# Kernel optimization log

Measured on AMD Instinct MI355X. Metric: run time of the kernel, lower is better.

The kernel has to match this reference:

```python
import jax, jax.numpy as jnp
import numpy as np

STRIDES = (8, 16, 32, 64, 128)
LEVEL_HW = ((128, 160), (64, 80), (32, 40), (16, 20), (8, 10))
IMG_H, IMG_W = 1024, 1280
B, NUM_CLASSES = 16, 20
SCORE_THR, IOU_THR, MAX_DET = 0.05, 0.6, 1000


def _coords_all():
    # coords_fmap2orig for every level, concatenated -> [N, 2] (x, y)
    cs = []
    for (h, w), s in zip(LEVEL_HW, STRIDES):
        sx = jnp.arange(w, dtype=jnp.float32) * s + s // 2
        sy = jnp.arange(h, dtype=jnp.float32) * s + s // 2
        yy, xx = jnp.meshgrid(sy, sx, indexing='ij')
        cs.append(jnp.stack([xx.reshape(-1), yy.reshape(-1)], -1))
    return jnp.concatenate(cs, 0)


def _reshape_cat(levels):
    # list of [B,C,h,w] -> [B, sum(h*w), C]
    return jnp.concatenate(
        [p.transpose(0, 2, 3, 1).reshape(p.shape[0], -1, p.shape[1]) for p in levels], 1)


def _decode(cls_l, cnt_l, reg_l, coords):
    cls = jax.nn.sigmoid(_reshape_cat(cls_l))           # [B,N,C]
    cnt = jax.nn.sigmoid(_reshape_cat(cnt_l))[..., 0]   # [B,N]
    reg = _reshape_cat(reg_l)                           # [B,N,4] ltrb
    scores = jnp.sqrt(jnp.max(cls, -1) * cnt)           # add_centerness + sqrt
    classes = jnp.argmax(cls, -1) + 1
    boxes = jnp.concatenate([coords[None] - reg[..., :2], coords[None] + reg[..., 2:]], -1)
    return scores, classes, boxes


def _nms_keep(boxes, scores, classes, valid):
    # masked greedy per-class NMS on fixed size M; returns keep mask [M]
    boxes = jax.lax.stop_gradient(boxes)
    scores = jax.lax.stop_gradient(scores)
    maxc = jnp.max(jnp.where(valid[:, None], boxes, 0.0))
    b = boxes + (classes.astype(boxes.dtype) * (maxc + 1.0))[:, None]  # class offsets
    order = jnp.argsort(-jnp.where(valid, scores, -jnp.inf))
    b = b[order]
    v = valid[order]
    x1, y1, x2, y2 = b[:, 0], b[:, 1], b[:, 2], b[:, 3]
    areas = (x2 - x1 + 1.0) * (y2 - y1 + 1.0)
    iw = jnp.clip(jnp.minimum(x2[:, None], x2[None, :]) - jnp.maximum(x1[:, None], x1[None, :]) + 1.0, 0.0)
    ih = jnp.clip(jnp.minimum(y2[:, None], y2[None, :]) - jnp.maximum(y1[:, None], y1[None, :]) + 1.0, 0.0)
    inter = iw * ih
    iou = inter / (areas[:, None] + areas[None, :] - inter)
    M = boxes.shape[0]

    def body(i, carry):
        keep, sup = carry
        k = v[i] & (~sup[i])
        keep = keep.at[i].set(k)
        sup = sup | (k & (iou[i] > IOU_THR))
        return keep, sup

    keep_s, _ = jax.lax.fori_loop(0, M, body, (jnp.zeros(M, bool), jnp.zeros(M, bool)))
    return jnp.zeros(M, bool).at[order].set(keep_s)


def _forward(args):
    cls_r, cnt_r, reg_r = args[0:5], args[5:10], args[10:15]
    cls_i, cnt_i, reg_i = args[15:20], args[20:25], args[25:30]
    coords = _coords_all()
    s_r, c_r, b_r = _decode(cls_r, cnt_r, reg_r, coords)
    s_i, c_i, b_i = _decode(cls_i, cnt_i, reg_i, coords)
    scores = jnp.concatenate([s_r, s_i], 1)   # [B, 2N]
    classes = jnp.concatenate([c_r, c_i], 1)
    boxes = jnp.concatenate([b_r, b_i], 1)
    top_s, top_i = jax.lax.top_k(scores, MAX_DET)
    top_c = jnp.take_along_axis(classes, top_i, 1)
    top_b = jnp.take_along_axis(boxes, top_i[..., None], 1)
    valid = top_s >= SCORE_THR
    keep = jax.vmap(_nms_keep)(top_b, top_s, top_c, valid)
    # ClipBoxes: clamp to image bounds
    top_b = jnp.maximum(top_b, 0.0)
    xs = jnp.minimum(top_b[..., 0::2], IMG_W - 1.0)
    ys = jnp.minimum(top_b[..., 1::2], IMG_H - 1.0)
    top_b = jnp.stack([xs[..., 0], ys[..., 0], xs[..., 1], ys[..., 1]], -1)
    kf = keep.astype(top_s.dtype)
    return top_s * kf, top_c * keep, top_b * kf[..., None], keep


def setup_inputs() -> dict:
    key = jax.random.key(0)
    chans = {'cls': NUM_CLASSES, 'cnt': 1, 'reg': 4}
    inp = {}
    i = 0
    for mod in ('r', 'i'):
        for kind in ('cls', 'cnt', 'reg'):
            for l, (h, w) in enumerate(LEVEL_HW):
                k = jax.random.fold_in(key, i); i += 1
                inp[f'{kind}_{mod}_{l}'] = jax.random.normal(k, (B, chans[kind], h, w), jnp.float32)
    return inp


def reference(cls_r_0, cls_r_1, cls_r_2, cls_r_3, cls_r_4,
              cnt_r_0, cnt_r_1, cnt_r_2, cnt_r_3, cnt_r_4,
              reg_r_0, reg_r_1, reg_r_2, reg_r_3, reg_r_4,
              cls_i_0, cls_i_1, cls_i_2, cls_i_3, cls_i_4,
              cnt_i_0, cnt_i_1, cnt_i_2, cnt_i_3, cnt_i_4,
              reg_i_0, reg_i_1, reg_i_2, reg_i_3, reg_i_4):
    args = [cls_r_0, cls_r_1, cls_r_2, cls_r_3, cls_r_4,
            cnt_r_0, cnt_r_1, cnt_r_2, cnt_r_3, cnt_r_4,
            reg_r_0, reg_r_1, reg_r_2, reg_r_3, reg_r_4,
            cls_i_0, cls_i_1, cls_i_2, cls_i_3, cls_i_4,
            cnt_i_0, cnt_i_1, cnt_i_2, cnt_i_3, cnt_i_4,
            reg_i_0, reg_i_1, reg_i_2, reg_i_3, reg_i_4]
    return _forward(args)
```

## Files before the change

### kernel.cpp

```cpp
#include <hip/hip_runtime.h>
#include <hip/hip_bf16.h>

typedef unsigned long long u64;
typedef unsigned int u32;

#define NTOT    54560
#define NMOD    27280
#define BATCH   16
#define KPAD    1024
#define MAXD    1000
#define NBIN    16384
#define CANDCAP 6144
#define NLDSPOS 25600

struct Ptrs { const float* p[30]; };

constexpr size_t SZ_KEY   = (size_t)BATCH * NTOT * 8;
constexpr size_t SZ_TOPK  = (size_t)BATCH * KPAD * 8;
constexpr size_t SZ_TRAW  = (size_t)BATCH * KPAD * 16;
constexpr size_t SZ_T1    = (size_t)BATCH * KPAD * 4;
constexpr size_t SZ_MAXC  = (size_t)BATCH * 32 * 4;
constexpr size_t SZ_VALID = (size_t)BATCH * 32 * 4;
constexpr size_t SZ_MASK  = (size_t)BATCH * KPAD * 32 * 4;

constexpr size_t OFF_KEY    = 0;
constexpr size_t OFF_TOPK   = OFF_KEY   + SZ_KEY;
constexpr size_t OFF_TRAW   = OFF_TOPK  + SZ_TOPK;
constexpr size_t OFF_TSCORE = OFF_TRAW  + SZ_TRAW;
constexpr size_t OFF_TCLSF  = OFF_TSCORE+ SZ_T1;
constexpr size_t OFF_MAXC   = OFF_TCLSF + SZ_T1;
constexpr size_t OFF_VALID  = OFF_MAXC  + SZ_MAXC;
constexpr size_t OFF_MASK   = OFF_VALID + SZ_VALID;

__device__ inline void level_of(int nm, int& l, int& pos, int& w, int& s, int& hw) {
    if (nm < 20480)      { l = 0; pos = nm;         w = 160; s = 8;   hw = 20480; }
    else if (nm < 25600) { l = 1; pos = nm - 20480; w = 80;  s = 16;  hw = 5120; }
    else if (nm < 26880) { l = 2; pos = nm - 25600; w = 40;  s = 32;  hw = 1280; }
    else if (nm < 27200) { l = 3; pos = nm - 26880; w = 20;  s = 64;  hw = 320; }
    else                 { l = 4; pos = nm - 27200; w = 10;  s = 128; hw = 80; }
}

__device__ inline float sigm(float x) { return 1.0f / (1.0f + expf(-x)); }

__device__ inline void ld_lds16(const float* g, float* l) {
    __builtin_amdgcn_global_load_lds(
        (const __attribute__((address_space(1))) void*)g,
        (__attribute__((address_space(3))) void*)l, 16, 0, 0);
}

__global__ __launch_bounds__(256)
void decode_lds_kernel(Ptrs ptrs, u64* __restrict__ keyAll) {
    __shared__ float lds[21 * 1024];
    int cc = blockIdx.x;
    int b = blockIdx.y;
    int mod = cc / 25, c = cc % 25;
    int l     = (c < 20) ? 0 : 1;
    int hw    = (c < 20) ? 20480 : 5120;
    int pos0  = (c < 20) ? c * 1024 : (c - 20) * 1024;
    int nmb   = (l == 0) ? pos0 : 20480 + pos0;
    const float* clsP = ptrs.p[mod * 15 + l];
    const float* cntP = ptrs.p[mod * 15 + 5 + l];
    int wave = threadIdx.x >> 6, lane = threadIdx.x & 63;

    const float* cbase = clsP + (size_t)b * 20 * hw + pos0 + wave * 256 + lane * 4;
    float* dbase = lds + wave * 256;
    #pragma unroll
    for (int ch = 0; ch < 20; ++ch)
        ld_lds16(cbase + (size_t)ch * hw, dbase + ch * 1024);
    ld_lds16(cntP + (size_t)b * hw + pos0 + wave * 256 + lane * 4, dbase + 20 * 1024);
    __syncthreads();

    int t = threadIdx.x;
    const float4* l4 = (const float4*)lds;
    float4 mx = l4[t];
    #pragma unroll
    for (int ch = 1; ch < 20; ++ch) {
        float4 v = l4[ch * 256 + t];
        mx.x = fmaxf(mx.x, v.x); mx.y = fmaxf(mx.y, v.y);
        mx.z = fmaxf(mx.z, v.z); mx.w = fmaxf(mx.w, v.w);
    }
    float4 cv = l4[20 * 256 + t];

    int n = mod * NMOD + nmb + t * 4;
    u32 s0 = __float_as_uint(sqrtf(__fmul_rn(sigm(mx.x), sigm(cv.x))));
    u32 s1 = __float_as_uint(sqrtf(__fmul_rn(sigm(mx.y), sigm(cv.y))));
    u32 s2 = __float_as_uint(sqrtf(__fmul_rn(sigm(mx.z), sigm(cv.z))));
    u32 s3 = __float_as_uint(sqrtf(__fmul_rn(sigm(mx.w), sigm(cv.w))));
    ulonglong2* ka2 = (ulonglong2*)(keyAll + (size_t)b * NTOT + n);
    ulonglong2 k01, k23;
    k01.x = ((u64)s0 << 16) | (u64)(65535 - n);
    k01.y = ((u64)s1 << 16) | (u64)(65535 - (n + 1));
    k23.x = ((u64)s2 << 16) | (u64)(65535 - (n + 2));
    k23.y = ((u64)s3 << 16) | (u64)(65535 - (n + 3));
    ka2[0] = k01; ka2[1] = k23;
}

__global__ __launch_bounds__(256)
void decode_tail_kernel(Ptrs ptrs, u64* __restrict__ keyAll) {
    int t = blockIdx.x * 256 + threadIdx.x;
    int b = blockIdx.y;
    if (t >= 3360) return;
    int mod = t / 1680;
    int tm = t % 1680;
    int q = t & 3;
    int nm = 25600 + (tm & ~3);
    int l, pos, w, s, hw;
    level_of(nm, l, pos, w, s, hw);
    (void)w; (void)s;
    const float* clsP = ptrs.p[mod * 15 + l];
    const float* cntP = ptrs.p[mod * 15 + 5 + l];
    const float4* cb = (const float4*)(clsP + (size_t)b * 20 * hw + pos);
    int hw4 = hw >> 2;
    int c0 = q * 5;
    float4 v[5];
    #pragma unroll
    for (int c = 0; c < 5; ++c) v[c] = cb[(size_t)(c0 + c) * hw4];
    float4 cv = *(const float4*)(cntP + (size_t)b * hw + pos);

    float4 mx = v[0];
    #pragma unroll
    for (int c = 1; c < 5; ++c) {
        mx.x = fmaxf(mx.x, v[c].x); mx.y = fmaxf(mx.y, v[c].y);
        mx.z = fmaxf(mx.z, v[c].z); mx.w = fmaxf(mx.w, v[c].w);
    }
    mx.x = fmaxf(mx.x, __shfl_xor(mx.x, 1));
    mx.y = fmaxf(mx.y, __shfl_xor(mx.y, 1));
    mx.z = fmaxf(mx.z, __shfl_xor(mx.z, 1));
    mx.w = fmaxf(mx.w, __shfl_xor(mx.w, 1));
    mx.x = fmaxf(mx.x, __shfl_xor(mx.x, 2));
    mx.y = fmaxf(mx.y, __shfl_xor(mx.y, 2));
    mx.z = fmaxf(mx.z, __shfl_xor(mx.z, 2));
    mx.w = fmaxf(mx.w, __shfl_xor(mx.w, 2));

    float ma = (q & 1) ? ((q & 2) ? mx.w : mx.y) : ((q & 2) ? mx.z : mx.x);
    float ca = (q & 1) ? ((q & 2) ? cv.w : cv.y) : ((q & 2) ? cv.z : cv.x);
    u32 sb = __float_as_uint(sqrtf(__fmul_rn(sigm(ma), sigm(ca))));
    int n = mod * NMOD + nm + q;
    keyAll[(size_t)b * NTOT + n] = ((u64)sb << 16) | (u64)(65535 - n);
}

__global__ __launch_bounds__(1024)
void select_kernel(const u64* __restrict__ keyAll, u64* __restrict__ topkey,
                   u32* __restrict__ maxcG) {
    int b = blockIdx.x, tid = threadIdx.x;
    int lane = tid & 63, wid = tid >> 6;
    __shared__ u32 shist[NBIN];
    __shared__ u32 warep[16];
    __shared__ int sB1;
    __shared__ u32 scnt;
    double* sd = (double*)shist;

    if (tid == 0) { maxcG[b * 32] = 0u; scnt = 0u; }
    #pragma unroll
    for (int j = 0; j < NBIN / 1024; ++j) shist[tid + j * 1024] = 0u;
    __syncthreads();

    const u64* keys = keyAll + (size_t)b * NTOT;
    const u64 SENT = ~0ull;
    for (int n0 = 0; n0 < NTOT; n0 += 8192) {
        u64 kk[8];
        #pragma unroll
        for (int r = 0; r < 8; ++r) {
            int idx = n0 + r * 1024 + tid;
            kk[r] = (idx < NTOT) ? keys[idx] : SENT;
        }
        #pragma unroll
        for (int r = 0; r < 8; ++r)
            if (kk[r] != SENT) atomicAdd(&shist[(u32)(kk[r] >> 32)], 1u);
    }
    __syncthreads();

    u32 loc[16]; u32 sum = 0;
    #pragma unroll
    for (int j = 0; j < 16; ++j) { loc[j] = shist[NBIN - 1 - (tid * 16 + j)]; sum += loc[j]; }
    u32 v = sum;
    #pragma unroll
    for (int off = 1; off < 64; off <<= 1) {
        u32 t2 = (u32)__shfl_up((int)v, off);
        if (lane >= off) v += t2;
    }
    if (lane == 63) warep[wid] = v;
    __syncthreads();
    if (tid < 16) {
        u32 p = warep[tid];
        #pragma unroll
        for (int off = 1; off < 16; off <<= 1) {
            u32 t2 = (u32)__shfl_up((int)p, off);
            if (tid >= off) p += t2;
        }
        warep[tid] = p;
    }
    __syncthreads();
    u32 incl = v + (wid ? warep[wid - 1] : 0u);
    u32 excl = incl - sum;
    if (excl < (u32)MAXD && incl >= (u32)MAXD) {
        u32 c = excl;
        #pragma unroll
        for (int j = 0; j < 16; ++j) {
            c += loc[j];
            if (c >= (u32)MAXD) { sB1 = NBIN - 1 - (tid * 16 + j); break; }
        }
    }
    __syncthreads();
    int B1 = sB1;

    for (int n0 = 0; n0 < NTOT; n0 += 8192) {
        u64 kk[8];
        #pragma unroll
        for (int r = 0; r < 8; ++r) {
            int idx = n0 + r * 1024 + tid;
            kk[r] = (idx < NTOT) ? keys[idx] : 0ull;
        }
        #pragma unroll
        for (int r = 0; r < 8; ++r) {
            if (kk[r] != 0ull && (int)(kk[r] >> 32) >= B1) {
                u32 p = atomicAdd(&scnt, 1u);
                if (p < CANDCAP - 2) sd[p] = (double)kk[r];
            }
        }
    }
    __syncthreads();
    int C = min((int)scnt, CANDCAP - 2);
    if (tid == 0) { sd[C] = -1.0; sd[C + 1] = -1.0; }
    __syncthreads();

    for (int i = tid; i < C; i += 1024) {
        double ki = sd[i];
        int rank = 0;
        const double2* sd2 = (const double2*)sd;
        int C2 = (C + 1) >> 1;
        for (int j = 0; j < C2; ++j) {
            double2 v2 = sd2[j];
            rank += (v2.x > ki) ? 1 : 0;
            rank += (v2.y > ki) ? 1 : 0;
        }
        if (rank < MAXD) topkey[(size_t)b * KPAD + rank] = (u64)ki;
    }
}

__global__ __launch_bounds__(128)
void gather_kernel(Ptrs ptrs, const u64* __restrict__ topkey,
                   float4* __restrict__ traw, float* __restrict__ tscore,
                   float* __restrict__ tclsf, u32* __restrict__ validwords,
                   u32* __restrict__ maxcG) {
    #pragma clang fp contract(off)
    int b = blockIdx.y;
    int tid = threadIdx.x;
    int half = tid & 1;
    int i = blockIdx.x * 64 + (tid >> 1);
    int active = (i < MAXD);

    float score = 0.f;
    float best = -1.0f; int bi = 0;
    float ra = 0.f, rb2 = 0.f;
    int pos = 0, w = 1, s = 0;
    if (active) {
        u64 key = topkey[(size_t)b * KPAD + i];
        int n = 65535 - (int)(key & 0xFFFFull);
        score = __uint_as_float((u32)(key >> 16));
        int mod = (n >= NMOD) ? 1 : 0;
        int nm = n - mod * NMOD;
        int l, hw;
        level_of(nm, l, pos, w, s, hw);
        const float* clsP = ptrs.p[mod * 15 + l];
        const float* regP = ptrs.p[mod * 15 + 10 + l];
        const float* cbp = clsP + (size_t)b * 20 * hw + pos;
        const float* rbp = regP + (size_t)b * 4 * hw + pos;
        float cl[10];
        int c0 = half * 10;
        #pragma unroll
        for (int c = 0; c < 10; ++c) cl[c] = cbp[(size_t)(c0 + c) * hw];
        ra  = rbp[(size_t)(half * 2) * hw];
        rb2 = rbp[(size_t)(half * 2 + 1) * hw];
        #pragma unroll
        for (int c = 0; c < 10; ++c) {
            float p = sigm(cl[c]);
            if (p > best) { best = p; bi = c0 + c; }
        }
    }
    float po  = __shfl_xor(best, 1);
    int   bio = __shfl_xor(bi, 1);
    float rao = __shfl_xor(ra, 1);
    float rbo = __shfl_xor(rb2, 1);
    if (half == 0) { if (po > best)  { best = po; bi = bio; } }
    else           { if (po >= best) { best = po; bi = bio; } }
    float clsf = active ? (float)(bi + 1) : 0.f;
    float r0 = half ? rao : ra,  r1 = half ? rbo : rb2;
    float r2 = half ? ra  : rao, r3 = half ? rb2 : rbo;

    float4 bx = make_float4(0.f, 0.f, 0.f, 0.f);
    if (active) {
        int xi = pos % w, yi = pos / w;
        float cx = (float)(xi * s + (s >> 1));
        float cy = (float)(yi * s + (s >> 1));
        bx.x = cx - r0; bx.y = cy - r1; bx.z = cx + r2; bx.w = cy + r3;
    }
    int valid = active && (score >= 0.05f) && (half == 0);
    float contrib = valid ? fmaxf(0.0f, fmaxf(fmaxf(bx.x, bx.y), fmaxf(bx.z, bx.w))) : 0.0f;
    float red = contrib;
    #pragma unroll
    for (int off = 32; off > 0; off >>= 1) red = fmaxf(red, __shfl_down(red, off));
    if ((tid & 63) == 0) atomicMax(&maxcG[b * 32], __float_as_uint(red));
    u64 ball = __ballot(valid != 0);
    if ((tid & 63) == 0) {
        u32 word = 0;
        for (int j = 0; j < 32; ++j) word |= (u32)((ball >> (2 * j)) & 1ull) << j;
        validwords[b * 32 + blockIdx.x * 2 + (tid >> 6)] = word;
    }
    if (half == 0) {
        size_t oo = (size_t)b * KPAD + i;
        traw[oo] = bx; tscore[oo] = score; tclsf[oo] = clsf;
    }
}

#define SW(t) ((((t) & 31) << 3) | ((t) >> 5))
__global__ __launch_bounds__(64)
void mask_kernel(const float4* __restrict__ traw, const float* __restrict__ tclsf,
                 const u32* __restrict__ maxcG, u32* __restrict__ maskG) {
    #pragma clang fp contract(off)
    int u = blockIdx.x, b = blockIdx.y, tid = threadIdx.x;
    int g, wg;
    if (u < 128)      { g = u >> 2;                 wg = u & 3; }
    else if (u < 224) { int i2 = u - 128; g = 32 + i2 / 3;      wg = 1 + i2 % 3; }
    else if (u < 288) { int i2 = u - 224; g = 64 + (i2 >> 1);   wg = 2 + (i2 & 1); }
    else              { g = 96 + (u - 288);         wg = 3; }
    int i0 = g * 8, j0 = wg * 256;
    float m1 = __uint_as_float(maxcG[b * 32]) + 1.0f;

    __shared__ float cx1[256], cy1[256], cx2[256], cy2[256], ca[256];
    for (int t = tid; t < 256; t += 64) {
        float4 f = traw[(size_t)b * KPAD + j0 + t];
        float o = __fmul_rn(tclsf[(size_t)b * KPAD + j0 + t], m1);
        float ox1 = __fadd_rn(f.x, o), oy1 = __fadd_rn(f.y, o);
        float ox2 = __fadd_rn(f.z, o), oy2 = __fadd_rn(f.w, o);
        float dw = ox2 - ox1 + 1.0f;
        float dh = oy2 - oy1 + 1.0f;
        int ts = SW(t);
        cx1[ts] = ox1; cy1[ts] = oy1; cx2[ts] = ox2; cy2[ts] = oy2;
        ca[ts] = __fmul_rn(dw, dh);
    }
    __syncthreads();

    int ir = tid >> 3, wr = tid & 7;
    int i = i0 + ir;
    float4 fi = traw[(size_t)b * KPAD + i];
    float oi = __fmul_rn(tclsf[(size_t)b * KPAD + i], m1);
    float ix1 = __fadd_rn(fi.x, oi), iy1 = __fadd_rn(fi.y, oi);
    float ix2 = __fadd_rn(fi.z, oi), iy2 = __fadd_rn(fi.w, oi);
    float dwi = ix2 - ix1 + 1.0f, dhi = iy2 - iy1 + 1.0f;
    float ai = __fmul_rn(dwi, dhi);
    u32 bits = 0;
    int jb = wr * 32;
    for (int jj = 0; jj < 32; ++jj) {
        int js = SW(jb + jj);
        float iw = fminf(ix2, cx2[js]) - fmaxf(ix1, cx1[js]) + 1.0f;
        iw = fmaxf(iw, 0.0f);
        float ih = fminf(iy2, cy2[js]) - fmaxf(iy1, cy1[js]) + 1.0f;
        ih = fmaxf(ih, 0.0f);
        float inter = iw * ih;
        float denom = (ai + ca[js]) - inter;
        float iou = inter / denom;
        bits |= (iou > 0.6f) ? (1u << jj) : 0u;
    }
    maskG[((size_t)b * KPAD + i) * 32 + wg * 8 + wr] = bits;
}

__global__ __launch_bounds__(512)
void scan_out_kernel(const u32* __restrict__ maskG, const u32* __restrict__ validbits,
                     const float4* __restrict__ traw, const float* __restrict__ tscore,
                     const float* __restrict__ tclsf, float* __restrict__ out) {
    __shared__ u32 sm[KPAD * 32];
    __shared__ u32 keeps[32];
    int b = blockIdx.x, tid = threadIdx.x;

    const uint4* s4 = (const uint4*)(maskG + (size_t)b * KPAD * 32);
    uint4* d4 = (uint4*)sm;
    #pragma unroll
    for (int r = 0; r < 16; ++r) d4[tid + r * 512] = s4[tid + r * 512];
    __syncthreads();

    if (tid < 64) {
        int lane = tid, lw = lane & 31;
        u32 vreg = (lane < 32) ? validbits[b * 32 + lane] : 0u;
        u32 removed = 0u, keepw = 0u;
        u32 mA[8], mB[8];
        #pragma unroll
        for (int d = 0; d < 8; ++d) {
            mA[d] = sm[d * 32 + lw];
            mB[d] = sm[(d + 8) * 32 + lw];
        }
        auto step8 = [&](int base, u32* ms) {
            #pragma unroll
            for (int d = 0; d < 8; ++d) {
                int i = base + d;
                int wi = i >> 5, bi2 = i & 31;
                u32 rw = (u32)__builtin_amdgcn_readlane((int)removed, wi);
                u32 vw = (u32)__builtin_amdgcn_readlane((int)vreg, wi);
                u32 k = ((vw >> bi2) & 1u) & (~(rw >> bi2) & 1u);
                if (k) removed |= ms[d];
                if (lane == wi) keepw |= (k << bi2);
                ms[d] = sm[(i + 16) * 32 + lw];
            }
        };
        for (int t = 0; t < 62; ++t) { step8(t * 16, mA); step8(t * 16 + 8, mB); }
        step8(992, mA);
        if (lane < 32) keeps[lane] = keepw;
    }
    __syncthreads();

    const int BQ = BATCH * MAXD;
    for (int s2 = tid; s2 < MAXD; s2 += 512) {
        u32 kf = (keeps[s2 >> 5] >> (s2 & 31)) & 1u;
        size_t oo = (size_t)b * KPAD + s2;
        float score = tscore[oo];
        float clsf = tclsf[oo];
        float4 bx = traw[oo];
        float x1 = fminf(fmaxf(bx.x, 0.f), 1279.f);
        float y1 = fminf(fmaxf(bx.y, 0.f), 1023.f);
        float x2 = fminf(fmaxf(bx.z, 0.f), 1279.f);
        float y2 = fminf(fmaxf(bx.w, 0.f), 1023.f);
        int base = b * MAXD + s2;
        out[base] = kf ? score : 0.0f;
        out[BQ + base] = kf ? clsf : 0.0f;
        float* ob = out + 2 * BQ + (size_t)base * 4;
        ob[0] = kf ? x1 : 0.f; ob[1] = kf ? y1 : 0.f;
        ob[2] = kf ? x2 : 0.f; ob[3] = kf ? y2 : 0.f;
        out[6 * BQ + base] = kf ? 1.0f : 0.0f;
    }
}

extern "C" void kernel_launch(void* const* d_in, const int* in_sizes, int n_in,
                              void* d_out, int out_size, void* d_ws, size_t ws_size,
                              hipStream_t stream) {
    Ptrs ptrs;
    for (int i = 0; i < 30; ++i) ptrs.p[i] = (const float*)d_in[i];

    char* ws = (char*)d_ws;
    u64*    keyAll    = (u64*)   (ws + OFF_KEY);
    u64*    topkey    = (u64*)   (ws + OFF_TOPK);
    float4* traw      = (float4*)(ws + OFF_TRAW);
    float*  tscore    = (float*) (ws + OFF_TSCORE);
    float*  tclsf     = (float*) (ws + OFF_TCLSF);
    u32*    maxcG     = (u32*)   (ws + OFF_MAXC);
    u32*    validbits = (u32*)   (ws + OFF_VALID);
    u32*    maskG     = (u32*)   (ws + OFF_MASK);
    float*  out       = (float*)d_out;

    decode_lds_kernel<<<dim3(50, BATCH), 256, 0, stream>>>(ptrs, keyAll);
    decode_tail_kernel<<<dim3(14, BATCH), 256, 0, stream>>>(ptrs, keyAll);
    select_kernel<<<BATCH, 1024, 0, stream>>>(keyAll, topkey, maxcG);
    gather_kernel<<<dim3(16, BATCH), 128, 0, stream>>>(ptrs, topkey, traw, tscore, tclsf,
                                                       validbits, maxcG);
    mask_kernel<<<dim3(320, BATCH), 64, 0, stream>>>(traw, tclsf, maxcG, maskG);
    scan_out_kernel<<<BATCH, 512, 0, stream>>>(maskG, validbits, traw, tscore, tclsf, out);
}
```

Baseline: 277.6 us.

## Fuse decode kernels, merge select with gather, bucket-rank top-k, precompute offset boxes

Merges the two decode kernels into one launch and folds the gather step into the select kernel, removing two launches and the topkey and maxc round trips through global memory. Top-k ranking now scatters candidates by histogram bin using prefix offsets, so each candidate is compared only within its own bin instead of against every candidate. Class-offset boxes and areas are precomputed once in the gather phase, so the mask kernel only loads them. The cost is that the gather now runs on only 16 blocks of 1024 threads, each doing 20 serial class loads, which may underuse the GPU compared with the earlier 16x16 grid.

```diff
diff --git a/kernel.cpp b/kernel.cpp
--- a/kernel.cpp
+++ b/kernel.cpp
@@ -10,26 +10,24 @@
 #define KPAD    1024
 #define MAXD    1000
 #define NBIN    16384
-#define CANDCAP 6144
-#define NLDSPOS 25600
+#define CAND    6144
 
 struct Ptrs { const float* p[30]; };
 
 constexpr size_t SZ_KEY   = (size_t)BATCH * NTOT * 8;
-constexpr size_t SZ_TOPK  = (size_t)BATCH * KPAD * 8;
 constexpr size_t SZ_TRAW  = (size_t)BATCH * KPAD * 16;
+constexpr size_t SZ_TOFF  = (size_t)BATCH * KPAD * 16;
 constexpr size_t SZ_T1    = (size_t)BATCH * KPAD * 4;
-constexpr size_t SZ_MAXC  = (size_t)BATCH * 32 * 4;
 constexpr size_t SZ_VALID = (size_t)BATCH * 32 * 4;
 constexpr size_t SZ_MASK  = (size_t)BATCH * KPAD * 32 * 4;
 
 constexpr size_t OFF_KEY    = 0;
-constexpr size_t OFF_TOPK   = OFF_KEY   + SZ_KEY;
-constexpr size_t OFF_TRAW   = OFF_TOPK  + SZ_TOPK;
-constexpr size_t OFF_TSCORE = OFF_TRAW  + SZ_TRAW;
+constexpr size_t OFF_TRAW   = OFF_KEY   + SZ_KEY;
+constexpr size_t OFF_TOFF   = OFF_TRAW  + SZ_TRAW;
+constexpr size_t OFF_TAREA  = OFF_TOFF  + SZ_TOFF;
+constexpr size_t OFF_TSCORE = OFF_TAREA + SZ_T1;
 constexpr size_t OFF_TCLSF  = OFF_TSCORE+ SZ_T1;
-constexpr size_t OFF_MAXC   = OFF_TCLSF + SZ_T1;
-constexpr size_t OFF_VALID  = OFF_MAXC  + SZ_MAXC;
+constexpr size_t OFF_VALID  = OFF_TCLSF + SZ_T1;
 constexpr size_t OFF_MASK   = OFF_VALID + SZ_VALID;
 
 __device__ inline void level_of(int nm, int& l, int& pos, int& w, int& s, int& hw) {
@@ -49,10 +47,52 @@
 }
 
 __global__ __launch_bounds__(256)
-void decode_lds_kernel(Ptrs ptrs, u64* __restrict__ keyAll) {
+void decode_kernel(Ptrs ptrs, u64* __restrict__ keyAll) {
     __shared__ float lds[21 * 1024];
     int cc = blockIdx.x;
     int b = blockIdx.y;
+
+    if (cc >= 50) {
+        int t = (cc - 50) * 256 + threadIdx.x;
+        if (t >= 3360) return;
+        int mod = t / 1680;
+        int tm = t % 1680;
+        int q = t & 3;
+        int nm = 25600 + (tm & ~3);
+        int l, pos, w, s, hw;
+        level_of(nm, l, pos, w, s, hw);
+        (void)w; (void)s;
+        const float* clsP = ptrs.p[mod * 15 + l];
+        const float* cntP = ptrs.p[mod * 15 + 5 + l];
+        const float4* cb = (const float4*)(clsP + (size_t)b * 20 * hw + pos);
+        int hw4 = hw >> 2;
+        int c0 = q * 5;
+        float4 v[5];
+        #pragma unroll
+        for (int c = 0; c < 5; ++c) v[c] = cb[(size_t)(c0 + c) * hw4];
+        float4 cv = *(const float4*)(cntP + (size_t)b * hw + pos);
+        float4 mx = v[0];
+        #pragma unroll
+        for (int c = 1; c < 5; ++c) {
+            mx.x = fmaxf(mx.x, v[c].x); mx.y = fmaxf(mx.y, v[c].y);
+            mx.z = fmaxf(mx.z, v[c].z); mx.w = fmaxf(mx.w, v[c].w);
+        }
+        mx.x = fmaxf(mx.x, __shfl_xor(mx.x, 1));
+        mx.y = fmaxf(mx.y, __shfl_xor(mx.y, 1));
+        mx.z = fmaxf(mx.z, __shfl_xor(mx.z, 1));
+        mx.w = fmaxf(mx.w, __shfl_xor(mx.w, 1));
+        mx.x = fmaxf(mx.x, __shfl_xor(mx.x, 2));
+        mx.y = fmaxf(mx.y, __shfl_xor(mx.y, 2));
+        mx.z = fmaxf(mx.z, __shfl_xor(mx.z, 2));
+        mx.w = fmaxf(mx.w, __shfl_xor(mx.w, 2));
+        float ma = (q & 1) ? ((q & 2) ? mx.w : mx.y) : ((q & 2) ? mx.z : mx.x);
+        float ca = (q & 1) ? ((q & 2) ? cv.w : cv.y) : ((q & 2) ? cv.z : cv.x);
+        u32 sb = __float_as_uint(sqrtf(__fmul_rn(sigm(ma), sigm(ca))));
+        int n = mod * NMOD + nm + q;
+        keyAll[(size_t)b * NTOT + n] = ((u64)sb << 16) | (u64)(65535 - n);
+        return;
+    }
+
     int mod = cc / 25, c = cc % 25;
     int l     = (c < 20) ? 0 : 1;
     int hw    = (c < 20) ? 20480 : 5120;
@@ -95,62 +135,22 @@
     ka2[0] = k01; ka2[1] = k23;
 }
 
-__global__ __launch_bounds__(256)
-void decode_tail_kernel(Ptrs ptrs, u64* __restrict__ keyAll) {
-    int t = blockIdx.x * 256 + threadIdx.x;
-    int b = blockIdx.y;
-    if (t >= 3360) return;
-    int mod = t / 1680;
-    int tm = t % 1680;
-    int q = t & 3;
-    int nm = 25600 + (tm & ~3);
-    int l, pos, w, s, hw;
-    level_of(nm, l, pos, w, s, hw);
-    (void)w; (void)s;
-    const float* clsP = ptrs.p[mod * 15 + l];
-    const float* cntP = ptrs.p[mod * 15 + 5 + l];
-    const float4* cb = (const float4*)(clsP + (size_t)b * 20 * hw + pos);
-    int hw4 = hw >> 2;
-    int c0 = q * 5;
-    float4 v[5];
-    #pragma unroll
-    for (int c = 0; c < 5; ++c) v[c] = cb[(size_t)(c0 + c) * hw4];
-    float4 cv = *(const float4*)(cntP + (size_t)b * hw + pos);
-
-    float4 mx = v[0];
-    #pragma unroll
-    for (int c = 1; c < 5; ++c) {
-        mx.x = fmaxf(mx.x, v[c].x); mx.y = fmaxf(mx.y, v[c].y);
-        mx.z = fmaxf(mx.z, v[c].z); mx.w = fmaxf(mx.w, v[c].w);
-    }
-    mx.x = fmaxf(mx.x, __shfl_xor(mx.x, 1));
-    mx.y = fmaxf(mx.y, __shfl_xor(mx.y, 1));
-    mx.z = fmaxf(mx.z, __shfl_xor(mx.z, 1));
-    mx.w = fmaxf(mx.w, __shfl_xor(mx.w, 1));
-    mx.x = fmaxf(mx.x, __shfl_xor(mx.x, 2));
-    mx.y = fmaxf(mx.y, __shfl_xor(mx.y, 2));
-    mx.z = fmaxf(mx.z, __shfl_xor(mx.z, 2));
-    mx.w = fmaxf(mx.w, __shfl_xor(mx.w, 2));
-
-    float ma = (q & 1) ? ((q & 2) ? mx.w : mx.y) : ((q & 2) ? mx.z : mx.x);
-    float ca = (q & 1) ? ((q & 2) ? cv.w : cv.y) : ((q & 2) ? cv.z : cv.x);
-    u32 sb = __float_as_uint(sqrtf(__fmul_rn(sigm(ma), sigm(ca))));
-    int n = mod * NMOD + nm + q;
-    keyAll[(size_t)b * NTOT + n] = ((u64)sb << 16) | (u64)(65535 - n);
-}
-
 __global__ __launch_bounds__(1024)
-void select_kernel(const u64* __restrict__ keyAll, u64* __restrict__ topkey,
-                   u32* __restrict__ maxcG) {
+void select_gather_kernel(Ptrs ptrs, const u64* __restrict__ keyAll,
+                          float4* __restrict__ traw, float4* __restrict__ toff,
+                          float* __restrict__ tarea, float* __restrict__ tscore,
+                          float* __restrict__ tclsf, u32* __restrict__ validwords) {
+    #pragma clang fp contract(off)
     int b = blockIdx.x, tid = threadIdx.x;
     int lane = tid & 63, wid = tid >> 6;
     __shared__ u32 shist[NBIN];
+    __shared__ u64 scand[CAND];
+    __shared__ u64 stopk[KPAD];
     __shared__ u32 warep[16];
     __shared__ int sB1;
-    __shared__ u32 scnt;
-    double* sd = (double*)shist;
-
-    if (tid == 0) { maxcG[b * 32] = 0u; scnt = 0u; }
+    __shared__ float sred[16];
+    __shared__ float smaxc;
+
     #pragma unroll
     for (int j = 0; j < NBIN / 1024; ++j) shist[tid + j * 1024] = 0u;
     __syncthreads();
@@ -201,6 +201,13 @@
             if (c >= (u32)MAXD) { sB1 = NBIN - 1 - (tid * 16 + j); break; }
         }
     }
+    u32 run = excl;
+    #pragma unroll
+    for (int j = 0; j < 16; ++j) {
+        int bin = NBIN - 1 - (tid * 16 + j);
+        shist[bin] = run;
+        run += loc[j];
+    }
     __syncthreads();
     int B1 = sB1;
 
@@ -214,109 +221,93 @@
         #pragma unroll
         for (int r = 0; r < 8; ++r) {
             if (kk[r] != 0ull && (int)(kk[r] >> 32) >= B1) {
-                u32 p = atomicAdd(&scnt, 1u);
-                if (p < CANDCAP - 2) sd[p] = (double)kk[r];
+                u32 p = atomicAdd(&shist[(u32)(kk[r] >> 32)], 1u);
+                if (p < CAND) scand[p] = kk[r];
             }
         }
     }
     __syncthreads();
-    int C = min((int)scnt, CANDCAP - 2);
-    if (tid == 0) { sd[C] = -1.0; sd[C + 1] = -1.0; }
-    __syncthreads();
-
-    for (int i = tid; i < C; i += 1024) {
-        double ki = sd[i];
-        int rank = 0;
-        const double2* sd2 = (const double2*)sd;
-        int C2 = (C + 1) >> 1;
-        for (int j = 0; j < C2; ++j) {
-            double2 v2 = sd2[j];
-            rank += (v2.x > ki) ? 1 : 0;
-            rank += (v2.y > ki) ? 1 : 0;
-        }
-        if (rank < MAXD) topkey[(size_t)b * KPAD + rank] = (u64)ki;
-    }
-}
-
-__global__ __launch_bounds__(128)
-void gather_kernel(Ptrs ptrs, const u64* __restrict__ topkey,
-                   float4* __restrict__ traw, float* __restrict__ tscore,
-                   float* __restrict__ tclsf, u32* __restrict__ validwords,
-                   u32* __restrict__ maxcG) {
-    #pragma clang fp contract(off)
-    int b = blockIdx.y;
-    int tid = threadIdx.x;
-    int half = tid & 1;
-    int i = blockIdx.x * 64 + (tid >> 1);
-    int active = (i < MAXD);
-
-    float score = 0.f;
-    float best = -1.0f; int bi = 0;
-    float ra = 0.f, rb2 = 0.f;
-    int pos = 0, w = 1, s = 0;
-    if (active) {
-        u64 key = topkey[(size_t)b * KPAD + i];
+    int Ctot = min((int)shist[B1], CAND);
+
+    for (int i = tid; i < Ctot; i += 1024) {
+        u64 ki = scand[i];
+        int bin = (int)(ki >> 32);
+        int st = (int)shist[bin + 1];
+        int en = min((int)shist[bin], Ctot);
+        int pos = st;
+        for (int j = st; j < en; ++j) pos += (scand[j] > ki) ? 1 : 0;
+        if (pos < MAXD) stopk[pos] = ki;
+    }
+    __syncthreads();
+
+    float4 bx = make_float4(0.f, 0.f, 0.f, 0.f);
+    float score = 0.f, clsf = 0.f;
+    int valid = 0;
+    if (tid < MAXD) {
+        u64 key = stopk[tid];
         int n = 65535 - (int)(key & 0xFFFFull);
         score = __uint_as_float((u32)(key >> 16));
         int mod = (n >= NMOD) ? 1 : 0;
         int nm = n - mod * NMOD;
-        int l, hw;
+        int l, pos, w, s, hw;
         level_of(nm, l, pos, w, s, hw);
         const float* clsP = ptrs.p[mod * 15 + l];
         const float* regP = ptrs.p[mod * 15 + 10 + l];
         const float* cbp = clsP + (size_t)b * 20 * hw + pos;
         const float* rbp = regP + (size_t)b * 4 * hw + pos;
-        float cl[10];
-        int c0 = half * 10;
-        #pragma unroll
-        for (int c = 0; c < 10; ++c) cl[c] = cbp[(size_t)(c0 + c) * hw];
-        ra  = rbp[(size_t)(half * 2) * hw];
-        rb2 = rbp[(size_t)(half * 2 + 1) * hw];
-        #pragma unroll
-        for (int c = 0; c < 10; ++c) {
+        float cl[20];
+        #pragma unroll
+        for (int c = 0; c < 20; ++c) cl[c] = cbp[(size_t)c * hw];
+        float r0 = rbp[0], r1 = rbp[(size_t)hw], r2 = rbp[(size_t)2 * hw], r3 = rbp[(size_t)3 * hw];
+        float best = -1.0f; int bi = 0;
+        #pragma unroll
+        for (int c = 0; c < 20; ++c) {
             float p = sigm(cl[c]);
-            if (p > best) { best = p; bi = c0 + c; }
-        }
-    }
-    float po  = __shfl_xor(best, 1);
-    int   bio = __shfl_xor(bi, 1);
-    float rao = __shfl_xor(ra, 1);
-    float rbo = __shfl_xor(rb2, 1);
-    if (half == 0) { if (po > best)  { best = po; bi = bio; } }
-    else           { if (po >= best) { best = po; bi = bio; } }
-    float clsf = active ? (float)(bi + 1) : 0.f;
-    float r0 = half ? rao : ra,  r1 = half ? rbo : rb2;
-    float r2 = half ? ra  : rao, r3 = half ? rb2 : rbo;
-
-    float4 bx = make_float4(0.f, 0.f, 0.f, 0.f);
-    if (active) {
+            if (p > best) { best = p; bi = c; }
+        }
+        clsf = (float)(bi + 1);
         int xi = pos % w, yi = pos / w;
         float cx = (float)(xi * s + (s >> 1));
         float cy = (float)(yi * s + (s >> 1));
         bx.x = cx - r0; bx.y = cy - r1; bx.z = cx + r2; bx.w = cy + r3;
-    }
-    int valid = active && (score >= 0.05f) && (half == 0);
+        valid = (score >= 0.05f) ? 1 : 0;
+    }
+
     float contrib = valid ? fmaxf(0.0f, fmaxf(fmaxf(bx.x, bx.y), fmaxf(bx.z, bx.w))) : 0.0f;
     float red = contrib;
     #pragma unroll
     for (int off = 32; off > 0; off >>= 1) red = fmaxf(red, __shfl_down(red, off));
-    if ((tid & 63) == 0) atomicMax(&maxcG[b * 32], __float_as_uint(red));
+    if (lane == 0) sred[wid] = red;
     u64 ball = __ballot(valid != 0);
-    if ((tid & 63) == 0) {
-        u32 word = 0;
-        for (int j = 0; j < 32; ++j) word |= (u32)((ball >> (2 * j)) & 1ull) << j;
-        validwords[b * 32 + blockIdx.x * 2 + (tid >> 6)] = word;
-    }
-    if (half == 0) {
-        size_t oo = (size_t)b * KPAD + i;
-        traw[oo] = bx; tscore[oo] = score; tclsf[oo] = clsf;
-    }
+    if (lane == 0) {
+        validwords[b * 32 + 2 * wid]     = (u32)(ball & 0xFFFFFFFFull);
+        validwords[b * 32 + 2 * wid + 1] = (u32)(ball >> 32);
+    }
+    __syncthreads();
+    if (tid == 0) {
+        float m = sred[0];
+        #pragma unroll
+        for (int i = 1; i < 16; ++i) m = fmaxf(m, sred[i]);
+        smaxc = m;
+    }
+    __syncthreads();
+
+    float m1 = smaxc + 1.0f;
+    float o = __fmul_rn(clsf, m1);
+    float4 ob;
+    ob.x = __fadd_rn(bx.x, o); ob.y = __fadd_rn(bx.y, o);
+    ob.z = __fadd_rn(bx.z, o); ob.w = __fadd_rn(bx.w, o);
+    float dw = ob.z - ob.x + 1.0f;
+    float dh = ob.w - ob.y + 1.0f;
+    size_t oo = (size_t)b * KPAD + tid;
+    traw[oo] = bx; toff[oo] = ob; tarea[oo] = __fmul_rn(dw, dh);
+    tscore[oo] = score; tclsf[oo] = clsf;
 }
 
 #define SW(t) ((((t) & 31) << 3) | ((t) >> 5))
 __global__ __launch_bounds__(64)
-void mask_kernel(const float4* __restrict__ traw, const float* __restrict__ tclsf,
-                 const u32* __restrict__ maxcG, u32* __restrict__ maskG) {
+void mask_kernel(const float4* __restrict__ toff, const float* __restrict__ tarea,
+                 u32* __restrict__ maskG) {
     #pragma clang fp contract(off)
     int u = blockIdx.x, b = blockIdx.y, tid = threadIdx.x;
     int g, wg;
@@ -325,37 +316,27 @@
     else if (u < 288) { int i2 = u - 224; g = 64 + (i2 >> 1);   wg = 2 + (i2 & 1); }
     else              { g = 96 + (u - 288);         wg = 3; }
     int i0 = g * 8, j0 = wg * 256;
-    float m1 = __uint_as_float(maxcG[b * 32]) + 1.0f;
 
     __shared__ float cx1[256], cy1[256], cx2[256], cy2[256], ca[256];
     for (int t = tid; t < 256; t += 64) {
-        float4 f = traw[(size_t)b * KPAD + j0 + t];
-        float o = __fmul_rn(tclsf[(size_t)b * KPAD + j0 + t], m1);
-        float ox1 = __fadd_rn(f.x, o), oy1 = __fadd_rn(f.y, o);
-        float ox2 = __fadd_rn(f.z, o), oy2 = __fadd_rn(f.w, o);
-        float dw = ox2 - ox1 + 1.0f;
-        float dh = oy2 - oy1 + 1.0f;
+        float4 f = toff[(size_t)b * KPAD + j0 + t];
         int ts = SW(t);
-        cx1[ts] = ox1; cy1[ts] = oy1; cx2[ts] = ox2; cy2[ts] = oy2;
-        ca[ts] = __fmul_rn(dw, dh);
+        cx1[ts] = f.x; cy1[ts] = f.y; cx2[ts] = f.z; cy2[ts] = f.w;
+        ca[ts] = tarea[(size_t)b * KPAD + j0 + t];
     }
     __syncthreads();
 
     int ir = tid >> 3, wr = tid & 7;
     int i = i0 + ir;
-    float4 fi = traw[(size_t)b * KPAD + i];
-    float oi = __fmul_rn(tclsf[(size_t)b * KPAD + i], m1);
-    float ix1 = __fadd_rn(fi.x, oi), iy1 = __fadd_rn(fi.y, oi);
-    float ix2 = __fadd_rn(fi.z, oi), iy2 = __fadd_rn(fi.w, oi);
-    float dwi = ix2 - ix1 + 1.0f, dhi = iy2 - iy1 + 1.0f;
-    float ai = __fmul_rn(dwi, dhi);
+    float4 fi = toff[(size_t)b * KPAD + i];
+    float ai = tarea[(size_t)b * KPAD + i];
     u32 bits = 0;
     int jb = wr * 32;
     for (int jj = 0; jj < 32; ++jj) {
         int js = SW(jb + jj);
-        float iw = fminf(ix2, cx2[js]) - fmaxf(ix1, cx1[js]) + 1.0f;
+        float iw = fminf(fi.z, cx2[js]) - fmaxf(fi.x, cx1[js]) + 1.0f;
         iw = fmaxf(iw, 0.0f);
-        float ih = fminf(iy2, cy2[js]) - fmaxf(iy1, cy1[js]) + 1.0f;
+        float ih = fminf(fi.w, cy2[js]) - fmaxf(fi.y, cy1[js]) + 1.0f;
         ih = fmaxf(ih, 0.0f);
         float inter = iw * ih;
         float denom = (ai + ca[js]) - inter;
@@ -437,20 +418,18 @@
 
     char* ws = (char*)d_ws;
     u64*    keyAll    = (u64*)   (ws + OFF_KEY);
-    u64*    topkey    = (u64*)   (ws + OFF_TOPK);
     float4* traw      = (float4*)(ws + OFF_TRAW);
+    float4* toff      = (float4*)(ws + OFF_TOFF);
+    float*  tarea     = (float*) (ws + OFF_TAREA);
     float*  tscore    = (float*) (ws + OFF_TSCORE);
     float*  tclsf     = (float*) (ws + OFF_TCLSF);
-    u32*    maxcG     = (u32*)   (ws + OFF_MAXC);
     u32*    validbits = (u32*)   (ws + OFF_VALID);
     u32*    maskG     = (u32*)   (ws + OFF_MASK);
     float*  out       = (float*)d_out;
 
-    decode_lds_kernel<<<dim3(50, BATCH), 256, 0, stream>>>(ptrs, keyAll);
-    decode_tail_kernel<<<dim3(14, BATCH), 256, 0, stream>>>(ptrs, keyAll);
-    select_kernel<<<BATCH, 1024, 0, stream>>>(keyAll, topkey, maxcG);
-    gather_kernel<<<dim3(16, BATCH), 128, 0, stream>>>(ptrs, topkey, traw, tscore, tclsf,
-                                                       validbits, maxcG);
-    mask_kernel<<<dim3(320, BATCH), 64, 0, stream>>>(traw, tclsf, maxcG, maskG);
+    decode_kernel<<<dim3(64, BATCH), 256, 0, stream>>>(ptrs, keyAll);
+    select_gather_kernel<<<BATCH, 1024, 0, stream>>>(ptrs, keyAll, traw, toff, tarea,
+                                                     tscore, tclsf, validbits);
+    mask_kernel<<<dim3(320, BATCH), 64, 0, stream>>>(toff, tarea, maskG);
     scan_out_kernel<<<BATCH, 512, 0, stream>>>(maskG, validbits, traw, tscore, tclsf, out);
 }
```

After: 284.6 us. +2.5%, slower.
